# Optimization experiments

Hardware: AMD Instinct MI355X
Metric: run time of the kernel (lower is better)

The kernel has to match this reference:

```python
import jax, jax.numpy as jnp
import numpy as np

N = 100000
E = 1600000
D = 128
EPS = 1e-5


def setup_inputs() -> dict:
    key = jax.random.key(0)
    ks = jax.random.split(key, 12)
    nf_mat = jax.random.normal(ks[0], (N, D), dtype=jnp.float32)
    row = jax.random.randint(ks[1], (E,), 0, N, dtype=jnp.int32)  # target nodes
    col = jax.random.randint(ks[2], (E,), 0, N, dtype=jnp.int32)  # source nodes
    edge_weight = jax.random.uniform(ks[3], (E,), dtype=jnp.float32)
    s = 1.0 / np.sqrt(D)
    W1 = jax.random.normal(ks[4], (D, D), dtype=jnp.float32) * s
    W2 = jax.random.normal(ks[5], (D, D), dtype=jnp.float32) * s
    W3 = jax.random.normal(ks[6], (D, D), dtype=jnp.float32) * s
    b1 = jnp.zeros((D,), jnp.float32)
    b2 = jnp.zeros((D,), jnp.float32)
    b3 = jnp.zeros((D,), jnp.float32)
    gamma1 = jnp.ones((D,), jnp.float32)
    beta1 = jnp.zeros((D,), jnp.float32)
    gamma2 = jnp.ones((D,), jnp.float32)
    beta2 = jnp.zeros((D,), jnp.float32)
    # coeffs[l] = polynomial coefficients c0..c_order; init near identity (c1=1) + noise
    coeffs = jax.random.normal(ks[7], (2, 5), dtype=jnp.float32) * 0.1
    coeffs = coeffs.at[:, 1].add(1.0)
    return {"nf_mat": nf_mat, "row": row, "col": col, "edge_weight": edge_weight,
            "W1": W1, "b1": b1, "W2": W2, "b2": b2, "W3": W3, "b3": b3,
            "gamma1": gamma1, "beta1": beta1, "gamma2": gamma2, "beta2": beta2,
            "coeffs": coeffs}


def _gcn_conv(x, W, b, row, col, ew):
    # GCNConv(normalize=False): linear transform then weighted sparse aggregation
    h = x @ W                                   # [N, D]
    msg = h[col] * ew[:, None]                  # gather sources [E, D]
    agg = jax.ops.segment_sum(msg, row, num_segments=N)  # scatter to targets
    return agg + b


def _batchnorm(x, gamma, beta):
    m = jnp.mean(x, axis=0)
    v = jnp.var(x, axis=0)
    return (x - m) * jax.lax.rsqrt(v + EPS) * gamma + beta


def _poly(x, c):
    # Horner: c[0] + c[1]*x + ... + c[order]*x^order  (order=4)
    acc = jnp.full_like(x, c[-1])
    for k in range(c.shape[0] - 2, -1, -1):
        acc = acc * x + c[k]
    return acc


def reference(nf_mat, row, col, edge_weight, W1, b1, W2, b2, W3, b3,
              gamma1, beta1, gamma2, beta2, coeffs):
    x = _gcn_conv(nf_mat, W1, b1, row, col, edge_weight)
    x = _batchnorm(x, gamma1, beta1)
    x = _poly(x, coeffs[0])
    # dropout: eval mode -> identity
    x = _gcn_conv(x, W2, b2, row, col, edge_weight)
    x = _batchnorm(x, gamma2, beta2)
    x = _poly(x, coeffs[1])
    x = _gcn_conv(x, W3, b3, row, col, edge_weight)
    return x
```

## Files before the change

### kernel.cpp

```cpp
#include <hip/hip_runtime.h>
#include <hip/hip_bf16.h>

#define DD 128

typedef _Float16 h8_t __attribute__((ext_vector_type(8)));
typedef _Float16 h4_t __attribute__((ext_vector_type(4)));
typedef unsigned short us8_t __attribute__((ext_vector_type(8)));
typedef float f4_t __attribute__((ext_vector_type(4)));
typedef unsigned long long u64;

__device__ inline float bf2f(unsigned short u) {
  union { unsigned int i; float f; } v;
  v.i = ((unsigned int)u) << 16;
  return v.f;
}

__device__ inline float sat(float v) {
  return fminf(fmaxf(v, -60000.f), 60000.f);
}

__device__ inline float ldf(const void* p, int i, int f32m) {
  return f32m ? ((const float*)p)[i] : bf2f(((const unsigned short*)p)[i]);
}


__global__ __launch_bounds__(256) void k_hist(const int* __restrict__ row,
                                              int* __restrict__ deg, int E, int N,
                                              const unsigned int* __restrict__ nf,
                                              int* __restrict__ flag) {
  if (blockIdx.x == gridDim.x - 1) {
    __shared__ int cnt;
    if (threadIdx.x == 0) cnt = 0;
    __syncthreads();
    int bad = 0;
#pragma unroll
    for (int k = 0; k < 8; ++k) {
      unsigned int w = nf[threadIdx.x * 8 + k];
#pragma unroll
      for (int h = 0; h < 2; ++h) {
        unsigned short us = (h == 0) ? (unsigned short)(w & 0xFFFF)
                                     : (unsigned short)(w >> 16);
        float v = bf2f(us);
        float av = fabsf(v);
        if (!(av <= 1e5f) || (av != 0.f && av < 1e-30f)) bad++;
      }
    }
    atomicAdd(&cnt, bad);
    __syncthreads();
    if (threadIdx.x == 0) *flag = (cnt > 200) ? 1 : 0;
    return;
  }
  int i = blockIdx.x * 256 + threadIdx.x;
  if (i < E) {
    int r = row[i];
    if ((unsigned)r < (unsigned)N) atomicAdd(&deg[r], 1);
  }
}

__global__ __launch_bounds__(256) void k_scan1(const int* __restrict__ deg,
                                               int* __restrict__ bsum, int n) {
  int i0 = blockIdx.x * 1024 + threadIdx.x * 4;
  int s = 0;
#pragma unroll
  for (int k = 0; k < 4; ++k) {
    int i = i0 + k;
    if (i < n) s += deg[i];
  }
#pragma unroll
  for (int d = 1; d < 64; d <<= 1) s += __shfl_xor(s, d, 64);
  __shared__ int ws[4];
  int lane = threadIdx.x & 63, w = threadIdx.x >> 6;
  if (lane == 0) ws[w] = s;
  __syncthreads();
  if (threadIdx.x == 0) bsum[blockIdx.x] = ws[0] + ws[1] + ws[2] + ws[3];
}

__global__ __launch_bounds__(1024) void k_scan2(int* __restrict__ bsum,
                                                int* __restrict__ offs,
                                                int nb, int n) {
  __shared__ int sh[1024];
  int tid = threadIdx.x;
  sh[tid] = (tid < nb) ? bsum[tid] : 0;
  __syncthreads();
  if (tid == 0) {
    int run = 0;
    for (int i = 0; i < nb; ++i) {
      int t = sh[i];
      sh[i] = run;
      run += t;
    }
    offs[n] = run;
  }
  __syncthreads();
  if (tid < nb) bsum[tid] = sh[tid];
}

__global__ __launch_bounds__(256) void k_scan3(const int* __restrict__ deg,
                                               const int* __restrict__ bsum,
                                               int* __restrict__ offs,
                                               int* __restrict__ cursor,
                                               int* __restrict__ bcur, int n) {
  int tid = threadIdx.x, lane = tid & 63, w = tid >> 6;
  int i0 = blockIdx.x * 1024 + tid * 4;
  int v0 = 0, v1 = 0, v2 = 0, v3 = 0;
  if (i0 + 3 < n) {
    v0 = deg[i0]; v1 = deg[i0 + 1]; v2 = deg[i0 + 2]; v3 = deg[i0 + 3];
  } else {
    if (i0 < n) v0 = deg[i0];
    if (i0 + 1 < n) v1 = deg[i0 + 1];
    if (i0 + 2 < n) v2 = deg[i0 + 2];
  }
  int s = v0 + v1 + v2 + v3;
  int sc = s;
#pragma unroll
  for (int d = 1; d < 64; d <<= 1) {
    int t = __shfl_up(sc, d, 64);
    if (lane >= d) sc += t;
  }
  __shared__ int ws[4];
  if (lane == 63) ws[w] = sc;
  __syncthreads();
  int wbase = 0;
  for (int x = 0; x < w; ++x) wbase += ws[x];
  int run = bsum[blockIdx.x] + wbase + (sc - s);
  if (i0 < n) {
    offs[i0] = run; cursor[i0] = run;
    if ((i0 & 511) == 0) bcur[i0 >> 9] = run;
    run += v0;
  }
  if (i0 + 1 < n) { offs[i0 + 1] = run; cursor[i0 + 1] = run; run += v1; }
  if (i0 + 2 < n) { offs[i0 + 2] = run; cursor[i0 + 2] = run; run += v2; }
  if (i0 + 3 < n) { offs[i0 + 3] = run; cursor[i0 + 3] = run; }
}


#define P1_T 4096
#define NBMAX 256
#define P2_CAP 12288

__global__ __launch_bounds__(256) void k_p1(const int* __restrict__ row,
                                            const int* __restrict__ col,
                                            const void* __restrict__ ew,
                                            int* __restrict__ bcur,
                                            u64* __restrict__ stage,
                                            int E, int N, int NB,
                                            const int* __restrict__ flag) {
  __shared__ int hist[NBMAX];
  __shared__ int basep[NBMAX];
  int f32m = *flag;
  int tid = threadIdx.x;
  int e0 = blockIdx.x * P1_T;
  if (tid < NB) hist[tid] = 0;
  __syncthreads();
#pragma unroll
  for (int k = 0; k < P1_T / 256; ++k) {
    int i = e0 + k * 256 + tid;
    if (i < E) {
      int r = row[i];
      if ((unsigned)r < (unsigned)N) atomicAdd(&hist[r >> 9], 1);
    }
  }
  __syncthreads();
  if (tid < NB) {
    int c = hist[tid];
    basep[tid] = c ? atomicAdd(&bcur[tid], c) : 0;
    hist[tid] = 0;
  }
  __syncthreads();
#pragma unroll
  for (int k = 0; k < P1_T / 256; ++k) {
    int i = e0 + k * 256 + tid;
    if (i < E) {
      int r = row[i];
      if ((unsigned)r < (unsigned)N) {
        int b = r >> 9;
        int loc = atomicAdd(&hist[b], 1);
        int pos = basep[b] + loc;
        int c = col[i];
        if ((unsigned)c >= (unsigned)N) c = 0;
        unsigned int wb = __float_as_uint(ldf(ew, i, f32m));
        u64 pk = ((u64)wb << 32) | (unsigned int)(c | ((r & 511) << 17));
        stage[pos] = pk;
      }
    }
  }
}

__global__ __launch_bounds__(256) void k_p2(const int* __restrict__ offs,
                                            const u64* __restrict__ stage,
                                            u64* __restrict__ rec, int N) {
  __shared__ int lcur[512];
  __shared__ u64 recbuf[P2_CAP];
  int b = blockIdx.x;
  int base = b << 9;
  int nend = base + 512;
  if (nend > N) nend = N;
  int nn = nend - base;
  int recbase = offs[base];
  int cnt = offs[nend] - recbase;
  for (int v = threadIdx.x; v < nn; v += 256) lcur[v] = offs[base + v] - recbase;
  __syncthreads();
  for (int j = threadIdx.x; j < cnt; j += 256) {
    u64 pk = stage[recbase + j];
    unsigned int lo = (unsigned int)pk;
    unsigned int wb = (unsigned int)(pk >> 32);
    int c = lo & 0x1FFFF;
    int rloc = (lo >> 17) & 511;
    int pos = atomicAdd(&lcur[rloc], 1);
    u64 out = ((u64)wb << 32) | (unsigned int)c;
    if (pos < P2_CAP) recbuf[pos] = out;
    else rec[recbase + pos] = out;
  }
  __syncthreads();
  int m = cnt < P2_CAP ? cnt : P2_CAP;
  for (int j = threadIdx.x; j < m; j += 256) rec[recbase + j] = recbuf[j];
}

__global__ __launch_bounds__(256) void k_fill(const int* __restrict__ row,
                                              const int* __restrict__ col,
                                              const void* __restrict__ ew,
                                              int* __restrict__ cursor,
                                              int2* __restrict__ rec, int E, int N,
                                              const int* __restrict__ flag) {
  int f32m = *flag;
  int i = blockIdx.x * 256 + threadIdx.x;
  if (i >= E) return;
  int r = row[i];
  if ((unsigned)r >= (unsigned)N) return;
  int p = atomicAdd(&cursor[r], 1);
  if ((unsigned)p >= (unsigned)E) return;
  int c = col[i];
  if ((unsigned)c >= (unsigned)N) c = 0;
  rec[p] = make_int2(c, __float_as_int(ldf(ew, i, f32m)));
}

__global__ __launch_bounds__(256) void k_cvt_w(const void* __restrict__ W1,
                                               const void* __restrict__ W2,
                                               const void* __restrict__ W3,
                                               _Float16* __restrict__ Wt,
                                               const int* __restrict__ flag) {
  int f32m = *flag;
  int i = blockIdx.x * 256 + threadIdx.x;
  if (i >= 3 * 16384) return;
  int l = i >> 14, o = i & 16383;
  int j = o & 7, lane = (o >> 3) & 63, kkt = o >> 9;
  int kk = kkt & 3, t = kkt >> 2;
  int k = kk * 32 + (lane >> 4) * 8 + j;
  int n = t * 16 + (lane & 15);
  const void* W = (l == 0) ? W1 : (l == 1 ? W2 : W3);
  Wt[i] = (_Float16)ldf(W, k * 128 + n, f32m);
}


__global__ __launch_bounds__(128) void k_bnprep(const float* __restrict__ pb,
                                                const void* __restrict__ gamma,
                                                const void* __restrict__ beta,
                                                const void* __restrict__ coeffs,
                                                int coff, float invN,
                                                float* __restrict__ bn,
                                                const int* __restrict__ flag) {
  int f32m = *flag;
  int c = threadIdx.x;
  float s = 0.f, s2 = 0.f;
#pragma unroll 8
  for (int p = 0; p < 64; ++p) {
    s += pb[p * 256 + c];
    s2 += pb[p * 256 + 128 + c];
  }
  float mn = s * invN;
  float var = fmaf(-mn, mn, s2 * invN);
  var = fmaxf(var, 0.0f);
  float inv = rsqrtf(var + 1e-5f);
  float g = ldf(gamma, c, f32m);
  float scv = g * inv;
  bn[c] = scv;
  bn[128 + c] = ldf(beta, c, f32m) - mn * scv;
  if (c < 5) bn[256 + c] = ldf(coeffs, coff + c, f32m);
}


template <int MODE>
__global__ __launch_bounds__(256) void k_gemm(const void* __restrict__ Xraw,
                                              const _Float16* __restrict__ Wt,
                                              _Float16* __restrict__ H, int nrows,
                                              const float* __restrict__ bn,
                                              const int* __restrict__ flag,
                                              float* __restrict__ pbz) {
  if (pbz != nullptr && blockIdx.x < 64)
    pbz[(blockIdx.x << 8) + threadIdx.x] = 0.f;
  int gw = (blockIdx.x * 256 + threadIdx.x) >> 6;
  int lane = threadIdx.x & 63;
  int r0 = gw << 4;
  if (r0 >= nrows) return;
  int m = lane & 15, q = lane >> 4;
  int rr = r0 + m;
  if (rr >= nrows) rr = nrows - 1;
  h8_t a[4];
  if (MODE == 0) {
    int f32m = *flag;
    if (f32m) {
      const float* X = (const float*)Xraw + (size_t)rr * DD + q * 8;
#pragma unroll
      for (int kk = 0; kk < 4; ++kk) {
        float4 u0 = *(const float4*)(X + kk * 32);
        float4 u1 = *(const float4*)(X + kk * 32 + 4);
        a[kk] = h8_t{(_Float16)u0.x, (_Float16)u0.y, (_Float16)u0.z, (_Float16)u0.w,
                     (_Float16)u1.x, (_Float16)u1.y, (_Float16)u1.z, (_Float16)u1.w};
      }
    } else {
      const unsigned short* X = (const unsigned short*)Xraw + (size_t)rr * DD + q * 8;
#pragma unroll
      for (int kk = 0; kk < 4; ++kk) {
        us8_t u = *(const us8_t*)(X + kk * 32);
        h8_t o;
#pragma unroll
        for (int j = 0; j < 8; ++j) o[j] = (_Float16)bf2f(u[j]);
        a[kk] = o;
      }
    }
  } else {
    const _Float16* X = (const _Float16*)Xraw + (size_t)rr * DD + q * 8;
    const float* scp = bn;
    const float* shp = bn + 128;
    float p0 = bn[256], p1 = bn[257], p2 = bn[258], p3 = bn[259], p4 = bn[260];
#pragma unroll
    for (int kk = 0; kk < 4; ++kk) {
      h8_t x = *(const h8_t*)(X + kk * 32);
      int c0 = kk * 32 + q * 8;
      float scv[8], shv[8];
      *(float4*)scv = *(const float4*)(scp + c0);
      *(float4*)(scv + 4) = *(const float4*)(scp + c0 + 4);
      *(float4*)shv = *(const float4*)(shp + c0);
      *(float4*)(shv + 4) = *(const float4*)(shp + c0 + 4);
      h8_t o;
#pragma unroll
      for (int j = 0; j < 8; ++j) {
        float xn = fmaf((float)x[j], scv[j], shv[j]);
        xn = fminf(fmaxf(xn, -100.f), 100.f);
        float h = p4;
        h = fmaf(h, xn, p3);
        h = fmaf(h, xn, p2);
        h = fmaf(h, xn, p1);
        h = fmaf(h, xn, p0);
        o[j] = (_Float16)h;
      }
      a[kk] = o;
    }
  }
  f4_t acc[8] = {};
#pragma unroll
  for (int kk = 0; kk < 4; ++kk) {
#pragma unroll
    for (int t = 0; t < 8; ++t) {
      h8_t b = *(const h8_t*)(Wt + (((t * 4 + kk) * 64 + lane) << 3));
      acc[t] = __builtin_amdgcn_mfma_f32_16x16x32_f16(a[kk], b, acc[t], 0, 0, 0);
    }
  }
#pragma unroll
  for (int t = 0; t < 8; ++t) {
#pragma unroll
    for (int r = 0; r < 4; ++r) {
      int orow = r0 + q * 4 + r;
      if (orow < nrows)
        H[(size_t)orow * DD + t * 16 + m] = (_Float16)sat(acc[t][r]);
    }
  }
}


template <int FINAL, int STATS>
__global__ __launch_bounds__(256) void k_agg(const _Float16* __restrict__ h,
                                             const int* __restrict__ offs,
                                             const int2* __restrict__ rec,
                                             const void* __restrict__ bias,
                                             void* __restrict__ outp, int n, int E,
                                             const int* __restrict__ flag,
                                             float* __restrict__ pb) {
  int f32m = *flag;
  int wid = threadIdx.x >> 6;
  int lane = threadIdx.x & 63;
  int sub = lane >> 4;
  int fl = lane & 15;
  const uint4* h128 = (const uint4*)h;
  float ss[8] = {}, ss2[8] = {};
  float bv[8];
  {
    int c0 = fl << 3;
#pragma unroll
    for (int k = 0; k < 8; ++k) bv[k] = ldf(bias, c0 + k, f32m);
  }
#pragma unroll 1
  for (int t = 0; t < 4; ++t) {
    int node = (blockIdx.x << 4) + (wid << 2) + t;
    bool act = node < n;
    int beg = 0, end = 0;
    if (act) {
      beg = offs[node];
      end = offs[node + 1];
      if (beg < 0) beg = 0;
      if (end > E) end = E;
    }
    float a8[8] = {};
    for (int base = beg; base < end; base += 64) {
      int mm = end - base;
      if (mm > 64) mm = 64;
      int c = 0, wb = 0;
      if (lane < mm) {
        int2 r = rec[base + lane];
        c = r.x;
        wb = r.y;
      }
#pragma unroll 4
      for (int j = 0; j < mm; j += 4) {
        int idx = j + sub;
        int cc = __shfl(c, idx);
        float ww = __int_as_float(__shfl(wb, idx));
        if ((unsigned)cc >= (unsigned)n) cc = 0;
        union { uint4 u; h8_t f; } cv;
        cv.u = h128[(size_t)cc * 16 + fl];
#pragma unroll
        for (int k = 0; k < 8; ++k) a8[k] = fmaf((float)cv.f[k], ww, a8[k]);
      }
    }
#pragma unroll
    for (int k = 0; k < 8; ++k) a8[k] += __shfl_xor(a8[k], 16);
#pragma unroll
    for (int k = 0; k < 8; ++k) a8[k] += __shfl_xor(a8[k], 32);
    if (lane < 16 && act) {
      float o[8];
#pragma unroll
      for (int k = 0; k < 8; ++k) o[k] = sat(a8[k] + bv[k]);
      if (FINAL) {
        float4 v0 = make_float4(o[0], o[1], o[2], o[3]);
        float4 v1 = make_float4(o[4], o[5], o[6], o[7]);
        ((float4*)outp)[(size_t)node * 32 + fl * 2] = v0;
        ((float4*)outp)[(size_t)node * 32 + fl * 2 + 1] = v1;
      } else {
        union { uint4 u; h8_t f; } cv;
#pragma unroll
        for (int k = 0; k < 8; ++k) cv.f[k] = (_Float16)o[k];
        ((uint4*)outp)[(size_t)node * 16 + fl] = cv.u;
      }
      if (STATS) {
#pragma unroll
        for (int k = 0; k < 8; ++k) {
          ss[k] += o[k];
          ss2[k] = fmaf(o[k], o[k], ss2[k]);
        }
      }
    }
  }
  if (STATS) {
    __shared__ float sh[4][256];
    if (lane < 16) {
      int c0 = fl << 3;
#pragma unroll
      for (int k = 0; k < 8; ++k) {
        sh[wid][c0 + k] = ss[k];
        sh[wid][128 + c0 + k] = ss2[k];
      }
    }
    __syncthreads();
    int tid = threadIdx.x;
    float v = sh[0][tid] + sh[1][tid] + sh[2][tid] + sh[3][tid];
    float* dst = pb + ((blockIdx.x & 63) << 8);
    atomicAdd(&dst[tid], v);
  }
}


extern "C" void kernel_launch(void* const* d_in, const int* in_sizes, int n_in,
                              void* d_out, int out_size, void* d_ws, size_t ws_size,
                              hipStream_t stream) {
  const void* nf = d_in[0];
  const int* row = (const int*)d_in[1];
  const int* col = (const int*)d_in[2];
  const void* ew = d_in[3];
  const void* W1 = d_in[4];
  const void* b1 = d_in[5];
  const void* W2 = d_in[6];
  const void* b2 = d_in[7];
  const void* W3 = d_in[8];
  const void* b3 = d_in[9];
  const void* g1 = d_in[10];
  const void* be1 = d_in[11];
  const void* g2 = d_in[12];
  const void* be2 = d_in[13];
  const void* coeffs = d_in[14];

  const int N = in_sizes[0] / DD;
  const int E = in_sizes[1];
  const int cstride = in_sizes[14] / 2;

  char* p = (char*)d_ws;
  auto alloc = [&](size_t bytes) {
    char* r = p;
    p += (bytes + 255) & ~(size_t)255;
    return r;
  };
  int* flag = (int*)alloc(256);
  float* bn = (float*)alloc(2048);
  float* pb = (float*)alloc(65536);
  int* bsum = (int*)alloc(4096);
  int* bcur = (int*)alloc(1024);
  _Float16* Wt = (_Float16*)alloc(3 * 16384 * 2);
  _Float16* H16 = (_Float16*)alloc((size_t)N * DD * 2);
  int* deg = (int*)alloc((size_t)N * 4);
  int* offs = (int*)alloc((size_t)(N + 1) * 4);
  int* cursor = (int*)alloc((size_t)N * 4);
  int2* rec = (int2*)alloc((size_t)E * 8);
  u64* stage = (u64*)alloc((size_t)E * 8);

  _Float16* OUT = (_Float16*)d_out;

  int eb = (E + 255) / 256;
  hipMemsetAsync(deg, 0, (size_t)N * 4, stream);
  k_hist<<<eb + 1, 256, 0, stream>>>(row, deg, E, N, (const unsigned int*)nf, flag);
  int nb = (N + 1023) / 1024;
  k_scan1<<<nb, 256, 0, stream>>>(deg, bsum, N);
  k_scan2<<<1, 1024, 0, stream>>>(bsum, offs, nb, N);
  k_scan3<<<nb, 256, 0, stream>>>(deg, bsum, offs, cursor, bcur, N);

  int NB = (N + 511) >> 9;
  if (NB <= NBMAX) {
    k_p1<<<(E + P1_T - 1) / P1_T, 256, 0, stream>>>(row, col, ew, bcur, stage, E, N,
                                                    NB, flag);
    k_p2<<<NB, 256, 0, stream>>>(offs, stage, (u64*)rec, N);
  } else {
    k_fill<<<eb, 256, 0, stream>>>(row, col, ew, cursor, rec, E, N, flag);
  }

  k_cvt_w<<<192, 256, 0, stream>>>(W1, W2, W3, Wt, flag);

  int gemm_blocks = ((N + 15) / 16 + 3) / 4;
  int agg_blocks = (N + 15) / 16;
  float invN = 1.0f / (float)N;

  const void* Bs[3] = {b1, b2, b3};
  const void* Gs[2] = {g1, g2};
  const void* Bes[2] = {be1, be2};

  k_gemm<0><<<gemm_blocks, 256, 0, stream>>>(nf, Wt, H16, N, bn, flag, pb);
  k_agg<0, 1><<<agg_blocks, 256, 0, stream>>>(H16, offs, rec, Bs[0], OUT, N, E, flag, pb);
  k_bnprep<<<1, 128, 0, stream>>>(pb, Gs[0], Bes[0], coeffs, 0, invN, bn, flag);

  k_gemm<1><<<gemm_blocks, 256, 0, stream>>>(OUT, Wt + 16384, H16, N, bn, flag, pb);
  k_agg<0, 1><<<agg_blocks, 256, 0, stream>>>(H16, offs, rec, Bs[1], OUT, N, E, flag, pb);
  k_bnprep<<<1, 128, 0, stream>>>(pb, Gs[1], Bes[1], coeffs, cstride, invN, bn, flag);

  k_gemm<1><<<gemm_blocks, 256, 0, stream>>>(OUT, Wt + 2 * 16384, H16, N, bn, flag, nullptr);
  k_agg<1, 0><<<agg_blocks, 256, 0, stream>>>(H16, offs, rec, Bs[2], d_out, N, E, flag, pb);
}
```

Measured before the change: 557.4 us.

## Replace per-node degree histogram and scans with bucket-level histogram and in-block offsets

The CSR build no longer counts degrees per node with global atomics or runs three scan kernels. It counts edges per 512-node bucket in shared memory and scans those counts in one small kernel. Each bucket block in the second pass then computes its own per-node counts and offsets in LDS and writes the offs array itself. This removes a large global-atomic histogram and several launches, at the cost of an extra read pass over the staging buffer inside the bucket kernel.

```diff
diff --git a/kernel.cpp b/kernel.cpp
--- a/kernel.cpp
+++ b/kernel.cpp
@@ -23,11 +23,15 @@
   return f32m ? ((const float*)p)[i] : bf2f(((const unsigned short*)p)[i]);
 }
 
-
-__global__ __launch_bounds__(256) void k_hist(const int* __restrict__ row,
-                                              int* __restrict__ deg, int E, int N,
-                                              const unsigned int* __restrict__ nf,
-                                              int* __restrict__ flag) {
+#define P1_T 4096
+#define NBMAX 256
+#define P2_CAP 12288
+
+
+__global__ __launch_bounds__(256) void k_bhist(const int* __restrict__ row,
+                                               int* __restrict__ bcnt, int E, int N,
+                                               const unsigned int* __restrict__ nf,
+                                               int* __restrict__ flag) {
   if (blockIdx.x == gridDim.x - 1) {
     __shared__ int cnt;
     if (threadIdx.x == 0) cnt = 0;
@@ -50,93 +54,53 @@
     if (threadIdx.x == 0) *flag = (cnt > 200) ? 1 : 0;
     return;
   }
-  int i = blockIdx.x * 256 + threadIdx.x;
-  if (i < E) {
-    int r = row[i];
-    if ((unsigned)r < (unsigned)N) atomicAdd(&deg[r], 1);
-  }
-}
-
-__global__ __launch_bounds__(256) void k_scan1(const int* __restrict__ deg,
-                                               int* __restrict__ bsum, int n) {
-  int i0 = blockIdx.x * 1024 + threadIdx.x * 4;
-  int s = 0;
-#pragma unroll
-  for (int k = 0; k < 4; ++k) {
-    int i = i0 + k;
-    if (i < n) s += deg[i];
-  }
-#pragma unroll
-  for (int d = 1; d < 64; d <<= 1) s += __shfl_xor(s, d, 64);
-  __shared__ int ws[4];
-  int lane = threadIdx.x & 63, w = threadIdx.x >> 6;
-  if (lane == 0) ws[w] = s;
-  __syncthreads();
-  if (threadIdx.x == 0) bsum[blockIdx.x] = ws[0] + ws[1] + ws[2] + ws[3];
-}
-
-__global__ __launch_bounds__(1024) void k_scan2(int* __restrict__ bsum,
-                                                int* __restrict__ offs,
-                                                int nb, int n) {
-  __shared__ int sh[1024];
+  __shared__ int hist[NBMAX];
   int tid = threadIdx.x;
-  sh[tid] = (tid < nb) ? bsum[tid] : 0;
+  if (tid < NBMAX) hist[tid] = 0;
+  __syncthreads();
+  int e0 = blockIdx.x * P1_T;
+#pragma unroll
+  for (int k = 0; k < P1_T / 256; ++k) {
+    int i = e0 + k * 256 + tid;
+    if (i < E) {
+      int r = row[i];
+      if ((unsigned)r < (unsigned)N) atomicAdd(&hist[r >> 9], 1);
+    }
+  }
+  __syncthreads();
+  if (tid < NBMAX) {
+    int c = hist[tid];
+    if (c) atomicAdd(&bcnt[tid], c);
+  }
+}
+
+__global__ __launch_bounds__(256) void k_bscan(const int* __restrict__ bcnt,
+                                               int* __restrict__ bbase,
+                                               int* __restrict__ bcur,
+                                               int* __restrict__ offs,
+                                               int NB, int N) {
+  __shared__ int sh[NBMAX + 1];
+  int tid = threadIdx.x;
+  sh[tid] = (tid < NB) ? bcnt[tid] : 0;
   __syncthreads();
   if (tid == 0) {
     int run = 0;
-    for (int i = 0; i < nb; ++i) {
+    for (int i = 0; i < NB; ++i) {
       int t = sh[i];
       sh[i] = run;
       run += t;
     }
-    offs[n] = run;
-  }
-  __syncthreads();
-  if (tid < nb) bsum[tid] = sh[tid];
-}
-
-__global__ __launch_bounds__(256) void k_scan3(const int* __restrict__ deg,
-                                               const int* __restrict__ bsum,
-                                               int* __restrict__ offs,
-                                               int* __restrict__ cursor,
-                                               int* __restrict__ bcur, int n) {
-  int tid = threadIdx.x, lane = tid & 63, w = tid >> 6;
-  int i0 = blockIdx.x * 1024 + tid * 4;
-  int v0 = 0, v1 = 0, v2 = 0, v3 = 0;
-  if (i0 + 3 < n) {
-    v0 = deg[i0]; v1 = deg[i0 + 1]; v2 = deg[i0 + 2]; v3 = deg[i0 + 3];
-  } else {
-    if (i0 < n) v0 = deg[i0];
-    if (i0 + 1 < n) v1 = deg[i0 + 1];
-    if (i0 + 2 < n) v2 = deg[i0 + 2];
-  }
-  int s = v0 + v1 + v2 + v3;
-  int sc = s;
-#pragma unroll
-  for (int d = 1; d < 64; d <<= 1) {
-    int t = __shfl_up(sc, d, 64);
-    if (lane >= d) sc += t;
-  }
-  __shared__ int ws[4];
-  if (lane == 63) ws[w] = sc;
-  __syncthreads();
-  int wbase = 0;
-  for (int x = 0; x < w; ++x) wbase += ws[x];
-  int run = bsum[blockIdx.x] + wbase + (sc - s);
-  if (i0 < n) {
-    offs[i0] = run; cursor[i0] = run;
-    if ((i0 & 511) == 0) bcur[i0 >> 9] = run;
-    run += v0;
-  }
-  if (i0 + 1 < n) { offs[i0 + 1] = run; cursor[i0 + 1] = run; run += v1; }
-  if (i0 + 2 < n) { offs[i0 + 2] = run; cursor[i0 + 2] = run; run += v2; }
-  if (i0 + 3 < n) { offs[i0 + 3] = run; cursor[i0 + 3] = run; }
-}
-
-
-#define P1_T 4096
-#define NBMAX 256
-#define P2_CAP 12288
+    sh[NB] = run;
+    offs[N] = run;
+  }
+  __syncthreads();
+  if (tid < NB) {
+    bbase[tid] = sh[tid];
+    bcur[tid] = sh[tid];
+  }
+  if (tid == 0) bbase[NB] = sh[NB];
+}
+
 
 __global__ __launch_bounds__(256) void k_p1(const int* __restrict__ row,
                                             const int* __restrict__ col,
@@ -186,34 +150,171 @@
   }
 }
 
-__global__ __launch_bounds__(256) void k_p2(const int* __restrict__ offs,
-                                            const u64* __restrict__ stage,
-                                            u64* __restrict__ rec, int N) {
-  __shared__ int lcur[512];
+
+__global__ __launch_bounds__(256) void k_p2n(const int* __restrict__ bbase,
+                                             const u64* __restrict__ stage,
+                                             u64* __restrict__ rec,
+                                             int* __restrict__ offs, int N) {
+  __shared__ int lcnt[512];
+  __shared__ int lex[512];
+  __shared__ int wsum[4];
   __shared__ u64 recbuf[P2_CAP];
   int b = blockIdx.x;
   int base = b << 9;
   int nend = base + 512;
   if (nend > N) nend = N;
   int nn = nend - base;
-  int recbase = offs[base];
-  int cnt = offs[nend] - recbase;
-  for (int v = threadIdx.x; v < nn; v += 256) lcur[v] = offs[base + v] - recbase;
-  __syncthreads();
-  for (int j = threadIdx.x; j < cnt; j += 256) {
+  int recbase = bbase[b];
+  int cnt = bbase[b + 1] - recbase;
+  int tid = threadIdx.x;
+  lcnt[tid] = 0;
+  lcnt[tid + 256] = 0;
+  __syncthreads();
+  for (int j = tid; j < cnt; j += 256) {
+    unsigned int lo = (unsigned int)stage[recbase + j];
+    atomicAdd(&lcnt[(lo >> 17) & 511], 1);
+  }
+  __syncthreads();
+  int v0 = lcnt[2 * tid], v1 = lcnt[2 * tid + 1];
+  int s = v0 + v1;
+  int sc = s;
+  int lane = tid & 63, w = tid >> 6;
+#pragma unroll
+  for (int d = 1; d < 64; d <<= 1) {
+    int t = __shfl_up(sc, d, 64);
+    if (lane >= d) sc += t;
+  }
+  if (lane == 63) wsum[w] = sc;
+  __syncthreads();
+  int wbase = 0;
+  for (int x = 0; x < w; ++x) wbase += wsum[x];
+  int run = wbase + (sc - s);
+  lex[2 * tid] = run;
+  lex[2 * tid + 1] = run + v0;
+  __syncthreads();
+  for (int v = tid; v < nn; v += 256) offs[base + v] = recbase + lex[v];
+  lcnt[tid] = lex[tid];
+  lcnt[tid + 256] = lex[tid + 256];
+  __syncthreads();
+  for (int j = tid; j < cnt; j += 256) {
     u64 pk = stage[recbase + j];
     unsigned int lo = (unsigned int)pk;
     unsigned int wb = (unsigned int)(pk >> 32);
     int c = lo & 0x1FFFF;
     int rloc = (lo >> 17) & 511;
-    int pos = atomicAdd(&lcur[rloc], 1);
+    int pos = atomicAdd(&lcnt[rloc], 1);
     u64 out = ((u64)wb << 32) | (unsigned int)c;
     if (pos < P2_CAP) recbuf[pos] = out;
     else rec[recbase + pos] = out;
   }
   __syncthreads();
   int m = cnt < P2_CAP ? cnt : P2_CAP;
-  for (int j = threadIdx.x; j < m; j += 256) rec[recbase + j] = recbuf[j];
+  for (int j = tid; j < m; j += 256) rec[recbase + j] = recbuf[j];
+}
+
+
+__global__ __launch_bounds__(256) void k_hist(const int* __restrict__ row,
+                                              int* __restrict__ deg, int E, int N,
+                                              const unsigned int* __restrict__ nf,
+                                              int* __restrict__ flag) {
+  if (blockIdx.x == gridDim.x - 1) {
+    __shared__ int cnt;
+    if (threadIdx.x == 0) cnt = 0;
+    __syncthreads();
+    int bad = 0;
+#pragma unroll
+    for (int k = 0; k < 8; ++k) {
+      unsigned int w = nf[threadIdx.x * 8 + k];
+#pragma unroll
+      for (int h = 0; h < 2; ++h) {
+        unsigned short us = (h == 0) ? (unsigned short)(w & 0xFFFF)
+                                     : (unsigned short)(w >> 16);
+        float v = bf2f(us);
+        float av = fabsf(v);
+        if (!(av <= 1e5f) || (av != 0.f && av < 1e-30f)) bad++;
+      }
+    }
+    atomicAdd(&cnt, bad);
+    __syncthreads();
+    if (threadIdx.x == 0) *flag = (cnt > 200) ? 1 : 0;
+    return;
+  }
+  int i = blockIdx.x * 256 + threadIdx.x;
+  if (i < E) {
+    int r = row[i];
+    if ((unsigned)r < (unsigned)N) atomicAdd(&deg[r], 1);
+  }
+}
+
+__global__ __launch_bounds__(256) void k_scan1(const int* __restrict__ deg,
+                                               int* __restrict__ bsum, int n) {
+  int i0 = blockIdx.x * 1024 + threadIdx.x * 4;
+  int s = 0;
+#pragma unroll
+  for (int k = 0; k < 4; ++k) {
+    int i = i0 + k;
+    if (i < n) s += deg[i];
+  }
+#pragma unroll
+  for (int d = 1; d < 64; d <<= 1) s += __shfl_xor(s, d, 64);
+  __shared__ int ws[4];
+  int lane = threadIdx.x & 63, w = threadIdx.x >> 6;
+  if (lane == 0) ws[w] = s;
+  __syncthreads();
+  if (threadIdx.x == 0) bsum[blockIdx.x] = ws[0] + ws[1] + ws[2] + ws[3];
+}
+
+__global__ __launch_bounds__(1024) void k_scan2(int* __restrict__ bsum,
+                                                int* __restrict__ offs,
+                                                int nb, int n) {
+  __shared__ int sh[1024];
+  int tid = threadIdx.x;
+  sh[tid] = (tid < nb) ? bsum[tid] : 0;
+  __syncthreads();
+  if (tid == 0) {
+    int run = 0;
+    for (int i = 0; i < nb; ++i) {
+      int t = sh[i];
+      sh[i] = run;
+      run += t;
+    }
+    offs[n] = run;
+  }
+  __syncthreads();
+  if (tid < nb) bsum[tid] = sh[tid];
+}
+
+__global__ __launch_bounds__(256) void k_scan3(const int* __restrict__ deg,
+                                               const int* __restrict__ bsum,
+                                               int* __restrict__ offs,
+                                               int* __restrict__ cursor, int n) {
+  int tid = threadIdx.x, lane = tid & 63, w = tid >> 6;
+  int i0 = blockIdx.x * 1024 + tid * 4;
+  int v0 = 0, v1 = 0, v2 = 0, v3 = 0;
+  if (i0 + 3 < n) {
+    v0 = deg[i0]; v1 = deg[i0 + 1]; v2 = deg[i0 + 2]; v3 = deg[i0 + 3];
+  } else {
+    if (i0 < n) v0 = deg[i0];
+    if (i0 + 1 < n) v1 = deg[i0 + 1];
+    if (i0 + 2 < n) v2 = deg[i0 + 2];
+  }
+  int s = v0 + v1 + v2 + v3;
+  int sc = s;
+#pragma unroll
+  for (int d = 1; d < 64; d <<= 1) {
+    int t = __shfl_up(sc, d, 64);
+    if (lane >= d) sc += t;
+  }
+  __shared__ int ws[4];
+  if (lane == 63) ws[w] = sc;
+  __syncthreads();
+  int wbase = 0;
+  for (int x = 0; x < w; ++x) wbase += ws[x];
+  int run = bsum[blockIdx.x] + wbase + (sc - s);
+  if (i0 < n)     { offs[i0] = run;     cursor[i0] = run;     run += v0; }
+  if (i0 + 1 < n) { offs[i0 + 1] = run; cursor[i0 + 1] = run; run += v1; }
+  if (i0 + 2 < n) { offs[i0 + 2] = run; cursor[i0 + 2] = run; run += v2; }
+  if (i0 + 3 < n) { offs[i0 + 3] = run; cursor[i0 + 3] = run; }
 }
 
 __global__ __launch_bounds__(256) void k_fill(const int* __restrict__ row,
@@ -502,6 +603,8 @@
   float* bn = (float*)alloc(2048);
   float* pb = (float*)alloc(65536);
   int* bsum = (int*)alloc(4096);
+  int* bcnt = (int*)alloc(1024);
+  int* bbase = (int*)alloc(1088);
   int* bcur = (int*)alloc(1024);
   _Float16* Wt = (_Float16*)alloc(3 * 16384 * 2);
   _Float16* H16 = (_Float16*)alloc((size_t)N * DD * 2);
@@ -513,20 +616,22 @@
 
   _Float16* OUT = (_Float16*)d_out;
 
-  int eb = (E + 255) / 256;
-  hipMemsetAsync(deg, 0, (size_t)N * 4, stream);
-  k_hist<<<eb + 1, 256, 0, stream>>>(row, deg, E, N, (const unsigned int*)nf, flag);
-  int nb = (N + 1023) / 1024;
-  k_scan1<<<nb, 256, 0, stream>>>(deg, bsum, N);
-  k_scan2<<<1, 1024, 0, stream>>>(bsum, offs, nb, N);
-  k_scan3<<<nb, 256, 0, stream>>>(deg, bsum, offs, cursor, bcur, N);
-
   int NB = (N + 511) >> 9;
+  int p1b = (E + P1_T - 1) / P1_T;
   if (NB <= NBMAX) {
-    k_p1<<<(E + P1_T - 1) / P1_T, 256, 0, stream>>>(row, col, ew, bcur, stage, E, N,
-                                                    NB, flag);
-    k_p2<<<NB, 256, 0, stream>>>(offs, stage, (u64*)rec, N);
+    hipMemsetAsync(bcnt, 0, 1024, stream);
+    k_bhist<<<p1b + 1, 256, 0, stream>>>(row, bcnt, E, N, (const unsigned int*)nf, flag);
+    k_bscan<<<1, 256, 0, stream>>>(bcnt, bbase, bcur, offs, NB, N);
+    k_p1<<<p1b, 256, 0, stream>>>(row, col, ew, bcur, stage, E, N, NB, flag);
+    k_p2n<<<NB, 256, 0, stream>>>(bbase, stage, (u64*)rec, offs, N);
   } else {
+    int eb = (E + 255) / 256;
+    hipMemsetAsync(deg, 0, (size_t)N * 4, stream);
+    k_hist<<<eb + 1, 256, 0, stream>>>(row, deg, E, N, (const unsigned int*)nf, flag);
+    int nb = (N + 1023) / 1024;
+    k_scan1<<<nb, 256, 0, stream>>>(deg, bsum, N);
+    k_scan2<<<1, 1024, 0, stream>>>(bsum, offs, nb, N);
+    k_scan3<<<nb, 256, 0, stream>>>(deg, bsum, offs, cursor, N);
     k_fill<<<eb, 256, 0, stream>>>(row, col, ew, cursor, rec, E, N, flag);
   }
 
```

Measured after the change: 501.6 us. 1.11x faster.
